# Kernel tuning notes

Measured on AMD Instinct MI355X. Metric: run time of the kernel, lower is better.

Reference implementation:

```python
import jax, jax.numpy as jnp
import numpy as np

EPS = 1e-5
AVG_D = 32.0


def setup_inputs() -> dict:
    key = jax.random.key(0)
    ks = jax.random.split(key, 12)
    Ns, Nd, E, D, K = 1_000_000, 100_000, 3_200_000, 16, 2
    Fs, Fd, V = 4, 4, 100_000
    F = Fd + K  # predictor fields
    inp = {}
    inp["Cat_src"] = jax.random.randint(ks[0], (Ns, Fs), 0, V)
    inp["Cat_dst"] = jax.random.randint(ks[1], (Nd, Fd), 0, V)
    inp["src_ids"] = jax.random.randint(ks[2], (E,), 0, Ns)
    inp["dst_ids"] = jax.random.randint(ks[3], (E,), 0, Nd)
    inp["label"] = jax.random.randint(ks[4], (Nd,), 0, 2)
    inp["w"] = jax.random.normal(ks[5], (V, D), dtype=jnp.float32) * 0.05
    inp["W_agg"] = jax.random.normal(ks[6], (K, 12 * D, D), dtype=jnp.float32) * 0.05
    inp["b_agg"] = jnp.zeros((K, D), jnp.float32)
    inp["w_lin"] = jax.random.normal(ks[7], (F * D,), dtype=jnp.float32) * 0.05
    inp["b_lin"] = jnp.zeros((1,), jnp.float32)
    inp["W1"] = jax.random.normal(ks[8], (F * D, 64), dtype=jnp.float32) * 0.05
    inp["b1"] = jnp.zeros((64,), jnp.float32)
    inp["W2"] = jax.random.normal(ks[9], (64, 32), dtype=jnp.float32) * 0.05
    inp["b2"] = jnp.zeros((32,), jnp.float32)
    inp["W3"] = jax.random.normal(ks[10], (32, 1), dtype=jnp.float32) * 0.05
    inp["b3"] = jnp.zeros((1,), jnp.float32)
    return inp


def reference(Cat_src, Cat_dst, src_ids, dst_ids, label, w, W_agg, b_agg,
              w_lin, b_lin, W1, b1, W2, b2, W3, b3):
    Nd = Cat_dst.shape[0]
    # --- node embedding: gather cat fields, RowEmb with modes [mean, max] -> [Ns, K, D]
    emb = w[Cat_src]                                      # [Ns, Fs, D]
    h_src = jnp.stack([emb.mean(1), emb.max(1)], axis=1)  # [Ns, K, D]
    # --- multi-aggregator message passing (copy_u + segment min/max/mean, std via mean of h^2)
    m = h_src[src_ids]                                    # [E, K, D]
    deg = jax.ops.segment_sum(jnp.ones(src_ids.shape, m.dtype), dst_ids, Nd)
    safe = jnp.maximum(deg, 1.0)[:, None, None]
    mean = jax.ops.segment_sum(m, dst_ids, Nd) / safe
    mean2 = jax.ops.segment_sum(m * m, dst_ids, Nd) / safe
    has = (deg > 0)[:, None, None]
    mn = jnp.where(has, jax.ops.segment_min(m, dst_ids, Nd), 0.0)
    mx = jnp.where(has, jax.ops.segment_max(m, dst_ids, Nd), 0.0)
    std = jnp.sqrt(jax.nn.relu(mean2 - mean * mean) + EPS)
    tmp = jnp.concatenate([mean, mn, mx, std], axis=-1)   # [Nd, K, 4D]
    # --- PNA degree scalers: identity / amplification / attenuation
    logd = jnp.log(deg + 1.0)
    log_avg = jnp.log(AVG_D + 1.0)
    amp = (logd / log_avg)[:, None, None]
    att = jnp.where(logd > 0, log_avg / jnp.maximum(logd, EPS), 0.0)[:, None, None]
    scaled = jnp.concatenate([tmp, tmp * amp, tmp * att], axis=-1)  # [Nd, K, 12D]
    mes = jnp.einsum('nkf,kfd->nkd', scaled, W_agg) + b_agg          # [Nd, K, D]
    # --- final block: concat dst cat embeddings with aggregated messages
    x = jnp.concatenate([w[Cat_dst], mes], axis=1)        # [Nd, F, D]
    # --- DeepFM predictor: linear + FM pairwise + deep MLP
    flat = x.reshape(Nd, -1)
    lin = flat @ w_lin + b_lin[0]
    s = x.sum(1)
    fm = 0.5 * ((s * s) - (x * x).sum(1)).sum(-1)
    h = jax.nn.relu(flat @ W1 + b1)
    h = jax.nn.relu(h @ W2 + b2)
    deep = (h @ W3 + b3)[:, 0]
    pred = jax.nn.sigmoid(lin + fm + deep)
    return (pred, label)
```

## Files before the change

### kernel.cpp

```cpp
#include <hip/hip_runtime.h>
#include <math.h>

#define EPSF 1e-5f
#define BSH  5
#define BSZ  32
#define MAXB 4096
#define SBH  9
#define MAXSB 256
#define TILE 4096
#define SEG  8
#define BCAP 1472
#define XPADS2 104
#define X2PADS 72
#define HISTB 512
#define NPACK 14336

typedef __attribute__((ext_vector_type(8))) short short8;
typedef __attribute__((ext_vector_type(4))) float float4v;

__device__ inline unsigned f2bf_rne(float x) {
    unsigned u = __float_as_uint(x);
    u += 0x7FFF + ((u >> 16) & 1);
    return u >> 16;
}
__device__ inline short bf16_of(float x) { return (short)f2bf_rne(x); }
__device__ inline float bf2f_lo(unsigned hv) { return __uint_as_float(hv << 16); }
__device__ inline float bf2f_hi(unsigned hv) { return __uint_as_float(hv & 0xFFFF0000u); }
__device__ inline float bf2f_s(ushort s) { return __uint_as_float((unsigned)s << 16); }

__global__ __launch_bounds__(256) void setup_all(
    int* bcount, int nb,
    const float* __restrict__ W_agg, const float* __restrict__ W1,
    const float* __restrict__ W2, ushort* __restrict__ wpack,
    const float* __restrict__ w, ushort* __restrict__ wb, int VD, int do_cast)
{
    int nzb = (nb + 255) >> 8;
    int bid = blockIdx.x;
    if (bid < nzb) {
        int i = bid * 256 + threadIdx.x;
        if (i < nb) bcount[i] = 0;
        return;
    }
    if (bid == nzb) {
        for (int it = threadIdx.x; it < 1792; it += 256) {
            if (it < 768) {
                int t_g = it >> 6; int rem = it & 63;
                int q = rem >> 4, col = rem & 15;
                int kvar = t_g / 6, t = t_g % 6;
                const float* src = W_agg + kvar * 3072 + (t * 32 + q * 8) * 16 + col;
                ushort* dst = wpack + (size_t)it * 8;
#pragma unroll
                for (int j = 0; j < 8; ++j) dst[j] = (ushort)f2bf_rne(src[j * 16]);
            } else if (it < 1536) {
                int i2 = it - 768;
                int t = i2 >> 8; int rem = i2 & 255;
                int q = rem >> 6, col = rem & 63;
                const float* src = W1 + (t * 32 + q * 8) * 64 + col;
                ushort* dst = wpack + 6144 + (size_t)i2 * 8;
#pragma unroll
                for (int j = 0; j < 8; ++j) dst[j] = (ushort)f2bf_rne(src[j * 64]);
            } else {
                int i2 = it - 1536;
                int t = i2 >> 7; int rem = i2 & 127;
                int q = rem >> 5, col = rem & 31;
                const float* src = W2 + (t * 32 + q * 8) * 32 + col;
                ushort* dst = wpack + 12288 + (size_t)i2 * 8;
#pragma unroll
                for (int j = 0; j < 8; ++j) dst[j] = (ushort)f2bf_rne(src[j * 32]);
            }
        }
        return;
    }
    if (!do_cast) return;
    int i4 = ((bid - nzb - 1) * 256 + threadIdx.x) * 4;
    if (i4 + 3 < VD) {
        float4 v = *(const float4*)(w + i4);
        ushort4 o;
        o.x = (ushort)f2bf_rne(v.x); o.y = (ushort)f2bf_rne(v.y);
        o.z = (ushort)f2bf_rne(v.z); o.w = (ushort)f2bf_rne(v.w);
        *(ushort4*)(wb + i4) = o;
    } else {
        for (int j = i4; j < VD; ++j) wb[j] = (ushort)f2bf_rne(w[j]);
    }
}

__global__ __launch_bounds__(256) void build_h(
    const int* __restrict__ Cat_src, const ushort* __restrict__ wb,
    unsigned* __restrict__ h, int Ns)
{
    int gid = blockIdx.x * 256 + threadIdx.x;
    int s = gid >> 4;
    if (s >= Ns) return;
    int lane = threadIdx.x & 63;
    int d = lane & 15;
    int c = Cat_src[s * 4 + (d & 3)];
    float vs = 0.f, vm = -INFINITY;
#pragma unroll
    for (int f = 0; f < 4; ++f) {
        int id = __shfl(c, (lane & 48) + f, 64);
        float a = bf2f_s(wb[id * 16 + d]);
        vs += a; vm = fmaxf(vm, a);
    }
    unsigned packed = f2bf_rne(vs * 0.25f) | (f2bf_rne(vm) << 16);
    __builtin_nontemporal_store(packed, &h[s * 16 + d]);
}

__global__ __launch_bounds__(256) void hist_fine(const int* __restrict__ dst_ids,
                                                 int* bcount, int E, int nb) {
    __shared__ int hsh[MAXB];
    for (int i = threadIdx.x; i < nb; i += 256) hsh[i] = 0;
    __syncthreads();
    int stride = HISTB * 256;
    for (int e = blockIdx.x * 256 + threadIdx.x; e < E; e += stride)
        atomicAdd(&hsh[dst_ids[e] >> BSH], 1);
    __syncthreads();
    for (int i = threadIdx.x; i < nb; i += 256) {
        int c = hsh[i];
        if (c) atomicAdd(&bcount[i], c);
    }
}

__global__ __launch_bounds__(256) void scan_buckets(const int* __restrict__ bcount,
                                                    int* bstart, int* sbcursor,
                                                    int* gcur, int nb) {
    __shared__ int lsum[256];
    int tid = threadIdx.x;
    int v[16];
    int s = 0;
#pragma unroll
    for (int j = 0; j < 16; ++j) {
        int idx = tid * 16 + j;
        v[j] = (idx < nb) ? bcount[idx] : 0;
        s += v[j];
    }
    lsum[tid] = s;
    __syncthreads();
    for (int off = 1; off < 256; off <<= 1) {
        int y = (tid >= off) ? lsum[tid - off] : 0;
        __syncthreads();
        lsum[tid] += y;
        __syncthreads();
    }
    int run = lsum[tid] - s;
    if (tid * 16 < nb) sbcursor[tid] = run;
#pragma unroll
    for (int j = 0; j < 16; ++j) {
        int idx = tid * 16 + j;
        if (idx < nb) { bstart[idx] = run; gcur[idx] = run; }
        run += v[j];
    }
}

__global__ __launch_bounds__(256) void scatter_sb(
    const int* __restrict__ src_ids, const int* __restrict__ dst_ids,
    int* sbcursor, unsigned* __restrict__ pairs1, int E, int nsb)
{
    __shared__ int cnt[MAXSB];
    __shared__ int base[MAXSB];
    int tid = threadIdx.x;
    int t0 = blockIdx.x * TILE;
    for (int i = tid; i < nsb; i += 256) cnt[i] = 0;
    __syncthreads();
    int rank[TILE / 256];
#pragma unroll
    for (int j = 0; j < TILE / 256; ++j) {
        int e = t0 + j * 256 + tid;
        rank[j] = (e < E) ? atomicAdd(&cnt[dst_ids[e] >> SBH], 1) : 0;
    }
    __syncthreads();
    for (int i = tid; i < nsb; i += 256) {
        int c = cnt[i];
        base[i] = c ? atomicAdd(&sbcursor[i], c) : 0;
    }
    __syncthreads();
#pragma unroll
    for (int j = 0; j < TILE / 256; ++j) {
        int e = t0 + j * 256 + tid;
        if (e < E) {
            int d = dst_ids[e];
            int sb = d >> SBH;
            pairs1[base[sb] + rank[j]] =
                ((unsigned)src_ids[e] << 9) | (unsigned)(d & 511);
        }
    }
}

__global__ __launch_bounds__(256) void scatter_fine(
    const unsigned* __restrict__ pairs1, const int* __restrict__ bstart,
    int* gcur, unsigned* __restrict__ pairs2, int nb, int nsb, int E)
{
    __shared__ int cnt[16];
    __shared__ int base[16];
    int S = blockIdx.x >> 3, seg = blockIdx.x & (SEG - 1);
    int tid = threadIdx.x;
    int sbs = bstart[S << 4];
    int sbe = (S == nsb - 1) ? E : bstart[(S + 1) << 4];
    int len = sbe - sbs;
    int per = (len + SEG - 1) / SEG;
    int s0 = sbs + seg * per;
    int s1 = s0 + per; if (s1 > sbe) s1 = sbe;
    if (tid < 16) cnt[tid] = 0;
    __syncthreads();
    int rank[12];
    unsigned pv[12];
    int nit = (s1 - s0 + 255) >> 8;
    if (nit > 12) nit = 12;
    for (int j = 0; j < nit; ++j) {
        int e = s0 + j * 256 + tid;
        if (e < s1) {
            unsigned p = __builtin_nontemporal_load(&pairs1[e]);
            pv[j] = p;
            rank[j] = atomicAdd(&cnt[(p >> 5) & 15], 1);
        }
    }
    __syncthreads();
    if (tid < 16) {
        int idx = (S << 4) + tid;
        int c = cnt[tid];
        base[tid] = (c && idx < nb) ? atomicAdd(&gcur[idx], c) : 0;
    }
    __syncthreads();
    for (int j = 0; j < nit; ++j) {
        int e = s0 + j * 256 + tid;
        if (e < s1) {
            unsigned p = pv[j];
            pairs2[base[(p >> 5) & 15] + rank[j]] = p;
        }
    }
}


__device__ inline void bucket_sort(const unsigned* __restrict__ pairs,
                                   int gbase, int cnt,
                                   unsigned* sp, int* hist, int* ofs, int* start,
                                   int tid)
{
    if (tid < BSZ) hist[tid] = 0;
    __syncthreads();
    for (int i = tid; i < cnt; i += 256)
        atomicAdd(&hist[__builtin_nontemporal_load(&pairs[gbase + i]) & (BSZ - 1)], 1);
    __syncthreads();
    if (tid < BSZ) ofs[tid] = hist[tid];
    __syncthreads();
    for (int off = 1; off < BSZ; off <<= 1) {
        int y = (tid < BSZ && tid >= off) ? ofs[tid - off] : 0;
        __syncthreads();
        if (tid < BSZ) ofs[tid] += y;
        __syncthreads();
    }
    if (tid < BSZ) {
        start[tid] = ofs[tid] - hist[tid];
        ofs[tid] = ofs[tid] - hist[tid];
    }
    __syncthreads();
    for (int i = tid; i < cnt; i += 256) {
        unsigned p = __builtin_nontemporal_load(&pairs[gbase + i]);
        int r = atomicAdd(&ofs[p & (BSZ - 1)], 1);
        sp[r] = p;
    }
    __syncthreads();
}

__device__ inline void emit_stats(float sum0, float sq0, float mn0, float mx0,
                                  float sum1, float sq1, float mn1, float mx1,
                                  int dg, int n, int lane, int sub,
                                  ushort* __restrict__ tmpb, int* __restrict__ deg_out)
{
#pragma unroll
    for (int off = 16; off <= 32; off <<= 1) {
        sum0 += __shfl_xor(sum0, off); sq0 += __shfl_xor(sq0, off);
        mn0 = fminf(mn0, __shfl_xor(mn0, off)); mx0 = fmaxf(mx0, __shfl_xor(mx0, off));
        sum1 += __shfl_xor(sum1, off); sq1 += __shfl_xor(sq1, off);
        mn1 = fminf(mn1, __shfl_xor(mn1, off)); mx1 = fmaxf(mx1, __shfl_xor(mx1, off));
    }
    float safe = fmaxf((float)dg, 1.f);
    float r = 1.f / safe;
    bool has = dg > 0;
    float mean0 = sum0 * r, mean1 = sum1 * r;
    float sd0 = sqrtf(fmaxf(sq0 * r - mean0 * mean0, 0.f) + EPSF);
    float sd1 = sqrtf(fmaxf(sq1 * r - mean1 * mean1, 0.f) + EPSF);
    float v0 = (sub == 0) ? mean0 : (sub == 1) ? (has ? mn0 : 0.f)
             : (sub == 2) ? (has ? mx0 : 0.f) : sd0;
    float v1 = (sub == 0) ? mean1 : (sub == 1) ? (has ? mn1 : 0.f)
             : (sub == 2) ? (has ? mx1 : 0.f) : sd1;
    ushort* tp = tmpb + (size_t)n * 128;
    tp[lane] = (ushort)f2bf_rne(v0);
    tp[64 + lane] = (ushort)f2bf_rne(v1);
    if (lane == 0) deg_out[n] = dg;
}

__global__ __launch_bounds__(256) void agg_from_h(
    const unsigned* __restrict__ h,
    const int* __restrict__ bstart, const int* __restrict__ bcount,
    const unsigned* __restrict__ pairs,
    ushort* __restrict__ tmpb, int* __restrict__ deg_out, int Nd)
{
    __shared__ unsigned sp[BCAP];
    __shared__ int hist[BSZ];
    __shared__ int ofs[BSZ];
    __shared__ int start[BSZ];
    int b = blockIdx.x, tid = threadIdx.x;
    int cnt = bcount[b];
    int gbase = bstart[b];
    if (cnt > BCAP) cnt = BCAP;
    bucket_sort(pairs, gbase, cnt, sp, hist, ofs, start, tid);

    int wv = tid >> 6, lane = tid & 63, sub = lane >> 4, d = lane & 15;
#pragma unroll 1
    for (int q = 0; q < 8; ++q) {
        int dl = wv * 8 + q;
        int n = b * BSZ + dl;
        if (n >= Nd) break;
        int st = start[dl], dg = hist[dl];
        float sum0 = 0.f, sq0 = 0.f, mn0 = INFINITY, mx0 = -INFINITY;
        float sum1 = 0.f, sq1 = 0.f, mn1 = INFINITY, mx1 = -INFINITY;
        int nt = (dg + 31) >> 5;
        for (int t = 0; t < nt; ++t) {
            int base = t * 32 + sub;
            unsigned hv[8];
#pragma unroll
            for (int j = 0; j < 8; ++j) {
                int e = base + j * 4;
                int ec = (e < dg) ? e : (dg - 1);
                unsigned p = sp[st + ec];
                hv[j] = h[(p >> 9) * 16 + d];
            }
#pragma unroll
            for (int j = 0; j < 8; ++j) {
                int e = base + j * 4;
                if (e < dg) {
                    float me = bf2f_lo(hv[j]);
                    float vm = bf2f_hi(hv[j]);
                    sum0 += me; sq0 += me * me;
                    mn0 = fminf(mn0, me); mx0 = fmaxf(mx0, me);
                    sum1 += vm; sq1 += vm * vm;
                    mn1 = fminf(mn1, vm); mx1 = fmaxf(mx1, vm);
                }
            }
        }
        emit_stats(sum0, sq0, mn0, mx0, sum1, sq1, mn1, mx1,
                   dg, n, lane, sub, tmpb, deg_out);
    }
}

__global__ __launch_bounds__(256) void agg_from_w(
    const int* __restrict__ Cat_src, const float* __restrict__ w,
    const ushort* __restrict__ wb, int use_bf,
    const int* __restrict__ bstart, const int* __restrict__ bcount,
    const unsigned* __restrict__ pairs,
    ushort* __restrict__ tmpb, int* __restrict__ deg_out, int Nd)
{
    __shared__ unsigned sp[BCAP];
    __shared__ int hist[BSZ];
    __shared__ int ofs[BSZ];
    __shared__ int start[BSZ];
    int b = blockIdx.x, tid = threadIdx.x;
    int cnt = bcount[b];
    int gbase = bstart[b];
    if (cnt > BCAP) cnt = BCAP;
    bucket_sort(pairs, gbase, cnt, sp, hist, ofs, start, tid);

    int wv = tid >> 6, lane = tid & 63, sub = lane >> 4, d = lane & 15;
#pragma unroll 1
    for (int q = 0; q < 8; ++q) {
        int dl = wv * 8 + q;
        int n = b * BSZ + dl;
        if (n >= Nd) break;
        int st = start[dl], dg = hist[dl];
        float sum0 = 0.f, sq0 = 0.f, mn0 = INFINITY, mx0 = -INFINITY;
        float sum1 = 0.f, sq1 = 0.f, mn1 = INFINITY, mx1 = -INFINITY;
        int nt = (dg + 3) >> 2;
        for (int t = 0; t < nt; ++t) {
            int e4 = t * 4 + sub;
            int ec = (e4 < dg) ? e4 : (dg - 1);
            unsigned p = sp[st + ec];
            int src = (int)(p >> 9);
            int cat = Cat_src[src * 4 + (d & 3)];
            float vs = 0.f, vm = -INFINITY;
            if (use_bf) {
#pragma unroll
                for (int f = 0; f < 4; ++f) {
                    int id = __shfl(cat, sub * 16 + f, 64);
                    float a = bf2f_s(wb[id * 16 + d]);
                    vs += a; vm = fmaxf(vm, a);
                }
            } else {
#pragma unroll
                for (int f = 0; f < 4; ++f) {
                    int id = __shfl(cat, sub * 16 + f, 64);
                    float a = w[id * 16 + d];
                    vs += a; vm = fmaxf(vm, a);
                }
            }
            if (e4 < dg) {
                float me = vs * 0.25f;
                sum0 += me; sq0 += me * me;
                mn0 = fminf(mn0, me); mx0 = fmaxf(mx0, me);
                sum1 += vm; sq1 += vm * vm;
                mn1 = fminf(mn1, vm); mx1 = fmaxf(mx1, vm);
            }
        }
        emit_stats(sum0, sq0, mn0, mx0, sum1, sq1, mn1, mx1,
                   dg, n, lane, sub, tmpb, deg_out);
    }
}

__global__ __launch_bounds__(256) void finalize_mfma(
    const int* __restrict__ Cat_dst, const int* __restrict__ label,
    const float* __restrict__ w, const ushort* __restrict__ wpack,
    const float* __restrict__ b_agg,
    const float* __restrict__ w_lin, const float* __restrict__ b_lin,
    const float* __restrict__ b1, const float* __restrict__ b2,
    const float* __restrict__ W3, const float* __restrict__ b3,
    const int* __restrict__ deg_arr, const ushort* __restrict__ tmpb,
    float* __restrict__ out, int Nd)
{
    __shared__ __align__(16) ushort sx[4][16 * XPADS2];
    __shared__ __align__(16) ushort sx2[4][16 * X2PADS];
    __shared__ float sdeep[4][16];

    int tid = threadIdx.x;
    int wv = tid >> 6, lane = tid & 63;
    int q = lane >> 4, m = lane & 15;
    int n0 = (blockIdx.x * 4 + wv) * 16;
    int n = n0 + m;
    int nc = (n < Nd) ? n : (Nd - 1);

    ushort* X = sx[wv];
    ushort* X2 = sx2[wv];

    float fdeg = (float)deg_arr[nc];
    float logd = logf(fdeg + 1.f);
    const float logavg = logf(33.0f);
    float amp = logd / logavg;
    float att = (logd > 0.f) ? (logavg / fmaxf(logd, EPSF)) : 0.f;
    float ampr[4], attr[4];
#pragma unroll
    for (int r = 0; r < 4; ++r) {
        ampr[r] = __shfl(amp, q * 4 + r, 64);
        attr[r] = __shfl(att, q * 4 + r, 64);
    }

    const ushort* tpn = tmpb + (size_t)nc * 128;
#pragma unroll
    for (int kvar = 0; kvar < 2; ++kvar) {
        short8 af0 = *(const short8*)(tpn + kvar * 64 + q * 8);
        short8 af1 = *(const short8*)(tpn + kvar * 64 + 32 + q * 8);
        float4v aI = {0.f,0.f,0.f,0.f}, aA = {0.f,0.f,0.f,0.f}, aT = {0.f,0.f,0.f,0.f};
#pragma unroll
        for (int sb = 0; sb < 3; ++sb) {
            short8 b0 = *(const short8*)(wpack +
                (size_t)(((kvar * 6 + sb * 2) * 4 + q) * 16 + m) * 8);
            short8 b1v = *(const short8*)(wpack +
                (size_t)(((kvar * 6 + sb * 2 + 1) * 4 + q) * 16 + m) * 8);
            if (sb == 0) {
                aI = __builtin_amdgcn_mfma_f32_16x16x32_bf16(af0, b0, aI, 0, 0, 0);
                aI = __builtin_amdgcn_mfma_f32_16x16x32_bf16(af1, b1v, aI, 0, 0, 0);
            } else if (sb == 1) {
                aA = __builtin_amdgcn_mfma_f32_16x16x32_bf16(af0, b0, aA, 0, 0, 0);
                aA = __builtin_amdgcn_mfma_f32_16x16x32_bf16(af1, b1v, aA, 0, 0, 0);
            } else {
                aT = __builtin_amdgcn_mfma_f32_16x16x32_bf16(af0, b0, aT, 0, 0, 0);
                aT = __builtin_amdgcn_mfma_f32_16x16x32_bf16(af1, b1v, aT, 0, 0, 0);
            }
        }
        float bias = b_agg[kvar * 16 + m];
#pragma unroll
        for (int r = 0; r < 4; ++r)
            X[(q * 4 + r) * XPADS2 + 64 + kvar * 16 + m] = (ushort)f2bf_rne(
                aI[r] + ampr[r] * aA[r] + attr[r] * aT[r] + bias);
    }
    {
        int nl = lane >> 2, fl = lane & 3;
        int nn = n0 + nl;
        int nnc = (nn < Nd) ? nn : (Nd - 1);
        int cid = Cat_dst[nnc * 4 + fl];
        const float4* R = (const float4*)(w + (size_t)cid * 16);
        float4 r0 = R[0], r1 = R[1], r2 = R[2], r3 = R[3];
        short8 o0, o1;
        o0[0] = bf16_of(r0.x); o0[1] = bf16_of(r0.y);
        o0[2] = bf16_of(r0.z); o0[3] = bf16_of(r0.w);
        o0[4] = bf16_of(r1.x); o0[5] = bf16_of(r1.y);
        o0[6] = bf16_of(r1.z); o0[7] = bf16_of(r1.w);
        o1[0] = bf16_of(r2.x); o1[1] = bf16_of(r2.y);
        o1[2] = bf16_of(r2.z); o1[3] = bf16_of(r2.w);
        o1[4] = bf16_of(r3.x); o1[5] = bf16_of(r3.y);
        o1[6] = bf16_of(r3.z); o1[7] = bf16_of(r3.w);
        ushort* xp = X + nl * XPADS2 + fl * 16;
        *(short8*)(xp) = o0;
        *(short8*)(xp + 8) = o1;
    }
    __syncthreads();

    float lin = 0.f, sq = 0.f;
    float sd[16];
#pragma unroll
    for (int u = 0; u < 16; ++u) sd[u] = 0.f;
    {
        const ushort* xp = X + m * XPADS2 + q * 16;
        const float* wl = w_lin + q * 16;
#pragma unroll
        for (int u = 0; u < 16; ++u) {
            float v = bf2f_s(xp[u]);
            lin += v * wl[u]; sq += v * v; sd[u] += v;
        }
    }
    if (q < 2) {
        const ushort* xp = X + m * XPADS2 + (4 + q) * 16;
        const float* wl = w_lin + (4 + q) * 16;
#pragma unroll
        for (int u = 0; u < 16; ++u) {
            float v = bf2f_s(xp[u]);
            lin += v * wl[u]; sq += v * v; sd[u] += v;
        }
    }
#pragma unroll
    for (int off = 16; off <= 32; off <<= 1) {
        lin += __shfl_xor(lin, off);
        sq  += __shfl_xor(sq, off);
#pragma unroll
        for (int u = 0; u < 16; ++u) sd[u] += __shfl_xor(sd[u], off);
    }
    float fm = 0.f;
#pragma unroll
    for (int u = 0; u < 16; ++u) fm += sd[u] * sd[u];
    fm = 0.5f * (fm - sq);

    short8 xa[3];
#pragma unroll
    for (int t = 0; t < 3; ++t)
        xa[t] = *(const short8*)(X + m * XPADS2 + t * 32 + q * 8);
#pragma unroll
    for (int nt = 0; nt < 4; ++nt) {
        float4v acc = {0.f, 0.f, 0.f, 0.f};
#pragma unroll
        for (int t = 0; t < 3; ++t) {
            short8 bf = *(const short8*)(wpack + 6144 +
                (size_t)((t * 4 + q) * 64 + nt * 16 + m) * 8);
            acc = __builtin_amdgcn_mfma_f32_16x16x32_bf16(xa[t], bf, acc, 0, 0, 0);
        }
        float bb = b1[nt * 16 + m];
#pragma unroll
        for (int r = 0; r < 4; ++r)
            X2[(q * 4 + r) * X2PADS + nt * 16 + m] =
                (ushort)f2bf_rne(fmaxf(acc[r] + bb, 0.f));
    }
    __syncthreads();

    short8 ha[2];
#pragma unroll
    for (int t = 0; t < 2; ++t)
        ha[t] = *(const short8*)(X2 + m * X2PADS + t * 32 + q * 8);
    float dp[4] = {0.f, 0.f, 0.f, 0.f};
#pragma unroll
    for (int nt = 0; nt < 2; ++nt) {
        float4v acc = {0.f, 0.f, 0.f, 0.f};
#pragma unroll
        for (int t = 0; t < 2; ++t) {
            short8 bf = *(const short8*)(wpack + 12288 +
                (size_t)((t * 4 + q) * 32 + nt * 16 + m) * 8);
            acc = __builtin_amdgcn_mfma_f32_16x16x32_bf16(ha[t], bf, acc, 0, 0, 0);
        }
        float bb = b2[nt * 16 + m];
        float w3 = W3[nt * 16 + m];
#pragma unroll
        for (int r = 0; r < 4; ++r)
            dp[r] += fmaxf(acc[r] + bb, 0.f) * w3;
    }
#pragma unroll
    for (int off = 1; off <= 8; off <<= 1) {
#pragma unroll
        for (int r = 0; r < 4; ++r) dp[r] += __shfl_xor(dp[r], off);
    }
    if (m < 4)
        sdeep[wv][q * 4 + m] = (m == 0) ? dp[0] : (m == 1) ? dp[1]
                             : (m == 2) ? dp[2] : dp[3];
    __syncthreads();
    float deep = sdeep[wv][m];

    if (q == 0 && n < Nd) {
        float z = lin + b_lin[0] + fm + deep + b3[0];
        float pred = 1.f / (1.f + expf(-z));
        out[n] = pred;
        out[Nd + n] = (float)label[n];
    }
}

extern "C" void kernel_launch(void* const* d_in, const int* in_sizes, int n_in,
                              void* d_out, int out_size, void* d_ws, size_t ws_size,
                              hipStream_t stream) {
    const int*   Cat_src = (const int*)d_in[0];
    const int*   Cat_dst = (const int*)d_in[1];
    const int*   src_ids = (const int*)d_in[2];
    const int*   dst_ids = (const int*)d_in[3];
    const int*   label   = (const int*)d_in[4];
    const float* w       = (const float*)d_in[5];
    const float* W_agg   = (const float*)d_in[6];
    const float* b_agg   = (const float*)d_in[7];
    const float* w_lin   = (const float*)d_in[8];
    const float* b_lin   = (const float*)d_in[9];
    const float* W1      = (const float*)d_in[10];
    const float* b1      = (const float*)d_in[11];
    const float* W2      = (const float*)d_in[12];
    const float* b2      = (const float*)d_in[13];
    const float* W3      = (const float*)d_in[14];
    const float* b3      = (const float*)d_in[15];

    int E  = in_sizes[2];
    int Nd = in_sizes[4];
    int Ns = in_sizes[0] / 4;
    int VD = in_sizes[5];
    int nb  = (Nd + BSZ - 1) >> BSH;
    int nsb = (nb + 15) >> 4;

    int* bcount   = (int*)d_ws;
    int* bstart   = bcount + MAXB;
    int* sbcursor = bstart + MAXB;
    int* gcur     = sbcursor + MAXSB;
    int* deg      = gcur + MAXB;
    unsigned* pairs1 = (unsigned*)(deg + Nd);
    unsigned* pairs2 = pairs1 + E;
    size_t off_tmp = (((size_t)(MAXB * 3 + MAXSB + Nd) + 2 * (size_t)E) * 4 + 255)
                     & ~(size_t)255;
    ushort* tmpb = (ushort*)((char*)d_ws + off_tmp);
    ushort* wpack = tmpb + (size_t)Nd * 128;
    ushort* w_bf16 = wpack + NPACK;
    unsigned* h  = (unsigned*)(w_bf16 + VD);

    size_t need_common = off_tmp + (size_t)Nd * 256 + (size_t)NPACK * 2;
    size_t need_A = need_common + (size_t)VD * 2;
    size_t need_B = need_A + (size_t)Ns * 64;
    int mode = (ws_size >= need_B) ? 2 : (ws_size >= need_A) ? 1 : 0;

    float* out = (float*)d_out;

    int nzb = (nb + 255) >> 8;
    int ncb = (mode >= 1) ? (VD / 4 + 255) / 256 : 0;
    hipLaunchKernelGGL(setup_all, dim3(nzb + 1 + ncb), dim3(256), 0, stream,
                       bcount, nb, W_agg, W1, W2, wpack, w, w_bf16, VD, mode >= 1);
    if (mode == 2) {
        int hb = (int)(((size_t)Ns * 16 + 255) / 256);
        hipLaunchKernelGGL(build_h, dim3(hb), dim3(256), 0, stream,
                           Cat_src, w_bf16, h, Ns);
    }
    hipLaunchKernelGGL(hist_fine, dim3(HISTB), dim3(256), 0, stream,
                       dst_ids, bcount, E, nb);
    hipLaunchKernelGGL(scan_buckets, dim3(1), dim3(256), 0, stream,
                       bcount, bstart, sbcursor, gcur, nb);
    hipLaunchKernelGGL(scatter_sb, dim3((E + TILE - 1) / TILE), dim3(256), 0, stream,
                       src_ids, dst_ids, sbcursor, pairs1, E, nsb);
    hipLaunchKernelGGL(scatter_fine, dim3(nsb * SEG), dim3(256), 0, stream,
                       pairs1, bstart, gcur, pairs2, nb, nsb, E);
    if (mode == 2) {
        hipLaunchKernelGGL(agg_from_h, dim3(nb), dim3(256), 0, stream,
                           h, bstart, bcount, pairs2, tmpb, deg, Nd);
    } else {
        hipLaunchKernelGGL(agg_from_w, dim3(nb), dim3(256), 0, stream,
                           Cat_src, w, w_bf16, mode, bstart, bcount, pairs2,
                           tmpb, deg, Nd);
    }
    hipLaunchKernelGGL(finalize_mfma, dim3((Nd + 63) / 64), dim3(256), 0, stream,
                       Cat_dst, label, w, wpack, b_agg, w_lin, b_lin,
                       b1, b2, W3, b3, deg, tmpb, out, Nd);
}
```

Baseline: 327.0 us.

## Replace histogram+scan with fixed-capacity bucket slots for edge binning

Drops the histogram and prefix-scan kernels and gives every super-bucket and fine bucket a fixed-capacity region (BCAP per bucket, 16*BCAP per super-bucket). Cursors are seeded in setup to i*capacity, and the scatter kernels write into those regions with bounds checks. The aggregation kernels read counts from the final cursors. This removes two launches and a full pass over dst_ids, at the cost of a larger workspace and silently dropping edges if a bucket overflows its capacity.

```diff
diff --git a/kernel.cpp b/kernel.cpp
--- a/kernel.cpp
+++ b/kernel.cpp
@@ -10,9 +10,9 @@
 #define TILE 4096
 #define SEG  8
 #define BCAP 1472
+#define SBCAP (16 * BCAP)
 #define XPADS2 104
 #define X2PADS 72
-#define HISTB 512
 #define NPACK 14336
 
 typedef __attribute__((ext_vector_type(8))) short short8;
@@ -29,19 +29,20 @@
 __device__ inline float bf2f_s(ushort s) { return __uint_as_float((unsigned)s << 16); }
 
 __global__ __launch_bounds__(256) void setup_all(
-    int* bcount, int nb,
+    int* sbcursor, int* gcur, int nb, int nsb,
     const float* __restrict__ W_agg, const float* __restrict__ W1,
     const float* __restrict__ W2, ushort* __restrict__ wpack,
     const float* __restrict__ w, ushort* __restrict__ wb, int VD, int do_cast)
 {
-    int nzb = (nb + 255) >> 8;
+    int nzc = (nb + 255) >> 8;
     int bid = blockIdx.x;
-    if (bid < nzb) {
+    if (bid < nzc) {
         int i = bid * 256 + threadIdx.x;
-        if (i < nb) bcount[i] = 0;
+        if (i < nb) gcur[i] = i * BCAP;
+        if (i < nsb) sbcursor[i] = i * SBCAP;
         return;
     }
-    if (bid == nzb) {
+    if (bid == nzc) {
         for (int it = threadIdx.x; it < 1792; it += 256) {
             if (it < 768) {
                 int t_g = it >> 6; int rem = it & 63;
@@ -72,7 +73,7 @@
         return;
     }
     if (!do_cast) return;
-    int i4 = ((bid - nzb - 1) * 256 + threadIdx.x) * 4;
+    int i4 = ((bid - nzc - 1) * 256 + threadIdx.x) * 4;
     if (i4 + 3 < VD) {
         float4 v = *(const float4*)(w + i4);
         ushort4 o;
@@ -105,52 +106,6 @@
     __builtin_nontemporal_store(packed, &h[s * 16 + d]);
 }
 
-__global__ __launch_bounds__(256) void hist_fine(const int* __restrict__ dst_ids,
-                                                 int* bcount, int E, int nb) {
-    __shared__ int hsh[MAXB];
-    for (int i = threadIdx.x; i < nb; i += 256) hsh[i] = 0;
-    __syncthreads();
-    int stride = HISTB * 256;
-    for (int e = blockIdx.x * 256 + threadIdx.x; e < E; e += stride)
-        atomicAdd(&hsh[dst_ids[e] >> BSH], 1);
-    __syncthreads();
-    for (int i = threadIdx.x; i < nb; i += 256) {
-        int c = hsh[i];
-        if (c) atomicAdd(&bcount[i], c);
-    }
-}
-
-__global__ __launch_bounds__(256) void scan_buckets(const int* __restrict__ bcount,
-                                                    int* bstart, int* sbcursor,
-                                                    int* gcur, int nb) {
-    __shared__ int lsum[256];
-    int tid = threadIdx.x;
-    int v[16];
-    int s = 0;
-#pragma unroll
-    for (int j = 0; j < 16; ++j) {
-        int idx = tid * 16 + j;
-        v[j] = (idx < nb) ? bcount[idx] : 0;
-        s += v[j];
-    }
-    lsum[tid] = s;
-    __syncthreads();
-    for (int off = 1; off < 256; off <<= 1) {
-        int y = (tid >= off) ? lsum[tid - off] : 0;
-        __syncthreads();
-        lsum[tid] += y;
-        __syncthreads();
-    }
-    int run = lsum[tid] - s;
-    if (tid * 16 < nb) sbcursor[tid] = run;
-#pragma unroll
-    for (int j = 0; j < 16; ++j) {
-        int idx = tid * 16 + j;
-        if (idx < nb) { bstart[idx] = run; gcur[idx] = run; }
-        run += v[j];
-    }
-}
-
 __global__ __launch_bounds__(256) void scatter_sb(
     const int* __restrict__ src_ids, const int* __restrict__ dst_ids,
     int* sbcursor, unsigned* __restrict__ pairs1, int E, int nsb)
@@ -179,22 +134,24 @@
         if (e < E) {
             int d = dst_ids[e];
             int sb = d >> SBH;
-            pairs1[base[sb] + rank[j]] =
-                ((unsigned)src_ids[e] << 9) | (unsigned)(d & 511);
+            int idx = base[sb] + rank[j];
+            if (idx < (sb + 1) * SBCAP)
+                pairs1[idx] = ((unsigned)src_ids[e] << 9) | (unsigned)(d & 511);
         }
     }
 }
 
 __global__ __launch_bounds__(256) void scatter_fine(
-    const unsigned* __restrict__ pairs1, const int* __restrict__ bstart,
-    int* gcur, unsigned* __restrict__ pairs2, int nb, int nsb, int E)
+    const unsigned* __restrict__ pairs1, const int* __restrict__ sbcursor,
+    int* gcur, unsigned* __restrict__ pairs2, int nb, int nsb)
 {
     __shared__ int cnt[16];
     __shared__ int base[16];
     int S = blockIdx.x >> 3, seg = blockIdx.x & (SEG - 1);
     int tid = threadIdx.x;
-    int sbs = bstart[S << 4];
-    int sbe = (S == nsb - 1) ? E : bstart[(S + 1) << 4];
+    int sbs = S * SBCAP;
+    int sbe = sbcursor[S];
+    if (sbe > sbs + SBCAP) sbe = sbs + SBCAP;
     int len = sbe - sbs;
     int per = (len + SEG - 1) / SEG;
     int s0 = sbs + seg * per;
@@ -215,16 +172,20 @@
     }
     __syncthreads();
     if (tid < 16) {
-        int idx = (S << 4) + tid;
+        int gb = (S << 4) + tid;
         int c = cnt[tid];
-        base[tid] = (c && idx < nb) ? atomicAdd(&gcur[idx], c) : 0;
+        base[tid] = (c && gb < nb) ? atomicAdd(&gcur[gb], c) : 0;
     }
     __syncthreads();
     for (int j = 0; j < nit; ++j) {
         int e = s0 + j * 256 + tid;
         if (e < s1) {
             unsigned p = pv[j];
-            pairs2[base[(p >> 5) & 15] + rank[j]] = p;
+            int fb = (p >> 5) & 15;
+            int gb = (S << 4) + fb;
+            int idx = base[fb] + rank[j];
+            if (idx < (gb + 1) * BCAP)
+                pairs2[idx] = p;
         }
     }
 }
@@ -290,8 +251,7 @@
 }
 
 __global__ __launch_bounds__(256) void agg_from_h(
-    const unsigned* __restrict__ h,
-    const int* __restrict__ bstart, const int* __restrict__ bcount,
+    const unsigned* __restrict__ h, const int* __restrict__ gcur,
     const unsigned* __restrict__ pairs,
     ushort* __restrict__ tmpb, int* __restrict__ deg_out, int Nd)
 {
@@ -300,9 +260,10 @@
     __shared__ int ofs[BSZ];
     __shared__ int start[BSZ];
     int b = blockIdx.x, tid = threadIdx.x;
-    int cnt = bcount[b];
-    int gbase = bstart[b];
+    int gbase = b * BCAP;
+    int cnt = gcur[b] - gbase;
     if (cnt > BCAP) cnt = BCAP;
+    if (cnt < 0) cnt = 0;
     bucket_sort(pairs, gbase, cnt, sp, hist, ofs, start, tid);
 
     int wv = tid >> 6, lane = tid & 63, sub = lane >> 4, d = lane & 15;
@@ -345,8 +306,7 @@
 
 __global__ __launch_bounds__(256) void agg_from_w(
     const int* __restrict__ Cat_src, const float* __restrict__ w,
-    const ushort* __restrict__ wb, int use_bf,
-    const int* __restrict__ bstart, const int* __restrict__ bcount,
+    const ushort* __restrict__ wb, int use_bf, const int* __restrict__ gcur,
     const unsigned* __restrict__ pairs,
     ushort* __restrict__ tmpb, int* __restrict__ deg_out, int Nd)
 {
@@ -355,9 +315,10 @@
     __shared__ int ofs[BSZ];
     __shared__ int start[BSZ];
     int b = blockIdx.x, tid = threadIdx.x;
-    int cnt = bcount[b];
-    int gbase = bstart[b];
+    int gbase = b * BCAP;
+    int cnt = gcur[b] - gbase;
     if (cnt > BCAP) cnt = BCAP;
+    if (cnt < 0) cnt = 0;
     bucket_sort(pairs, gbase, cnt, sp, hist, ofs, start, tid);
 
     int wv = tid >> 6, lane = tid & 63, sub = lane >> 4, d = lane & 15;
@@ -613,14 +574,13 @@
     int nb  = (Nd + BSZ - 1) >> BSH;
     int nsb = (nb + 15) >> 4;
 
-    int* bcount   = (int*)d_ws;
-    int* bstart   = bcount + MAXB;
-    int* sbcursor = bstart + MAXB;
+    int* sbcursor = (int*)d_ws;
     int* gcur     = sbcursor + MAXSB;
     int* deg      = gcur + MAXB;
     unsigned* pairs1 = (unsigned*)(deg + Nd);
-    unsigned* pairs2 = pairs1 + E;
-    size_t off_tmp = (((size_t)(MAXB * 3 + MAXSB + Nd) + 2 * (size_t)E) * 4 + 255)
+    unsigned* pairs2 = pairs1 + (size_t)nsb * SBCAP;
+    size_t off_tmp = (((size_t)(MAXSB + MAXB + Nd)
+                      + (size_t)nsb * SBCAP + (size_t)nb * BCAP) * 4 + 255)
                      & ~(size_t)255;
     ushort* tmpb = (ushort*)((char*)d_ws + off_tmp);
     ushort* wpack = tmpb + (size_t)Nd * 128;
@@ -634,29 +594,26 @@
 
     float* out = (float*)d_out;
 
-    int nzb = (nb + 255) >> 8;
+    int nzc = (nb + 255) >> 8;
     int ncb = (mode >= 1) ? (VD / 4 + 255) / 256 : 0;
-    hipLaunchKernelGGL(setup_all, dim3(nzb + 1 + ncb), dim3(256), 0, stream,
-                       bcount, nb, W_agg, W1, W2, wpack, w, w_bf16, VD, mode >= 1);
+    hipLaunchKernelGGL(setup_all, dim3(nzc + 1 + ncb), dim3(256), 0, stream,
+                       sbcursor, gcur, nb, nsb, W_agg, W1, W2, wpack,
+                       w, w_bf16, VD, mode >= 1);
     if (mode == 2) {
         int hb = (int)(((size_t)Ns * 16 + 255) / 256);
         hipLaunchKernelGGL(build_h, dim3(hb), dim3(256), 0, stream,
                            Cat_src, w_bf16, h, Ns);
     }
-    hipLaunchKernelGGL(hist_fine, dim3(HISTB), dim3(256), 0, stream,
-                       dst_ids, bcount, E, nb);
-    hipLaunchKernelGGL(scan_buckets, dim3(1), dim3(256), 0, stream,
-                       bcount, bstart, sbcursor, gcur, nb);
     hipLaunchKernelGGL(scatter_sb, dim3((E + TILE - 1) / TILE), dim3(256), 0, stream,
                        src_ids, dst_ids, sbcursor, pairs1, E, nsb);
     hipLaunchKernelGGL(scatter_fine, dim3(nsb * SEG), dim3(256), 0, stream,
-                       pairs1, bstart, gcur, pairs2, nb, nsb, E);
+                       pairs1, sbcursor, gcur, pairs2, nb, nsb);
     if (mode == 2) {
         hipLaunchKernelGGL(agg_from_h, dim3(nb), dim3(256), 0, stream,
-                           h, bstart, bcount, pairs2, tmpb, deg, Nd);
+                           h, gcur, pairs2, tmpb, deg, Nd);
     } else {
         hipLaunchKernelGGL(agg_from_w, dim3(nb), dim3(256), 0, stream,
-                           Cat_src, w, w_bf16, mode, bstart, bcount, pairs2,
+                           Cat_src, w, w_bf16, mode, gcur, pairs2,
                            tmpb, deg, Nd);
     }
     hipLaunchKernelGGL(finalize_mfma, dim3((Nd + 63) / 64), dim3(256), 0, stream,
```

Result: faster. 295.9 us (-9.5%).
